# Performance work log

Hardware: AMD Instinct MI355X
Metric: run time of the kernel (lower is better)

## Reference

```python
import jax, jax.numpy as jnp
import numpy as np

B, N, M = 2, 4096, 12288
K, SH, H, GK, NC, F = 64, 32, 64, 8, 200, 1


def sph_to_cart(theta, phi):
    st = jnp.sin(theta)
    return jnp.stack([st * jnp.cos(phi), st * jnp.sin(phi), jnp.cos(theta)], axis=-1)


def setup_inputs() -> dict:
    key = jax.random.key(0)
    ks = jax.random.split(key, 16)
    theta = jax.random.uniform(ks[0], (B, N)) * jnp.pi
    phi = jax.random.uniform(ks[1], (B, N)) * 2 * jnp.pi
    feat = jax.random.normal(ks[2], (B, N))
    xxx = jnp.stack([theta, phi, feat], axis=1)  # [B,3,N]
    pt = jax.random.uniform(ks[3], (M,)) * jnp.pi
    pp = jax.random.uniform(ks[4], (M,)) * 2 * jnp.pi
    pix_theta_phi = jnp.stack([pt, pp], axis=1)  # [M,2]
    s = 0.1
    return dict(
        xxx=xxx,
        pix_theta_phi=pix_theta_phi,
        att_w1=jax.random.normal(ks[5], (F + 1, SH)) * s,
        att_b1=jnp.zeros((SH,)),
        att_w2=jax.random.normal(ks[6], (SH, 1)) * s,
        att_b2=jnp.zeros((1,)),
        proj_w=jax.random.normal(ks[7], (F, H)) * s,
        proj_b=jnp.zeros((H,)),
        rel_w=jax.random.normal(ks[8], (3, H, H)) * s,
        rel_b=jnp.zeros((3, H)),
        root_w=jax.random.normal(ks[9], (3, H, H)) * s,
        out_w1=jax.random.normal(ks[10], (H, H)) * s,
        out_b1=jnp.zeros((H,)),
        out_w2=jax.random.normal(ks[11], (H, NC)) * s,
        out_b2=jnp.zeros((NC,)),
    )


def reference(xxx, pix_theta_phi, att_w1, att_b1, att_w2, att_b2, proj_w, proj_b,
              rel_w, rel_b, root_w, out_w1, out_b1, out_w2, out_b2):
    # --- sparse healpix sampler ---
    los_tp = jnp.transpose(xxx[:, :2, :], (0, 2, 1))   # [B,N,2]
    x = xxx[:, 2, :][..., None]                        # [B,N,1]
    r_los = sph_to_cart(los_tp[..., 0], los_tp[..., 1])           # [B,N,3]
    r_pix = sph_to_cart(pix_theta_phi[:, 0], pix_theta_phi[:, 1])  # [M,3]
    cos = jnp.clip(jnp.einsum('bnc,mc->bmn', r_los, r_pix), -1.0, 1.0)  # [B,M,N]
    vals, idx = jax.lax.top_k(cos, K)                  # [B,M,K]
    x_g = jax.vmap(lambda xb, ib: xb[ib])(x, idx)      # [B,M,K,F]
    d = jnp.arccos(jnp.clip(vals, -1.0, 1.0))          # [B,M,K]
    feat = jnp.concatenate([x_g, d[..., None]], axis=-1)  # [B,M,K,F+1]
    logits = jax.nn.relu(feat @ att_w1 + att_b1) @ att_w2 + att_b2  # [B,M,K,1]
    w = jax.nn.softmax(logits[..., 0], axis=-1)        # [B,M,K]
    pooled = jnp.einsum('bmk,bmkf->bmf', w, x_g)       # [B,M,F]
    # --- GNN on healpix grid ---
    h = jax.nn.relu(pooled @ proj_w + proj_b)          # [B,M,H]
    m = r_pix.shape[0]
    sq = jnp.sum(r_pix * r_pix, axis=1)
    d2 = sq[:, None] + sq[None, :] - 2.0 * (r_pix @ r_pix.T)       # [M,M]
    d2 = jnp.where(jnp.eye(m, dtype=bool), jnp.inf, d2)  # loop=False
    _, nbr = jax.lax.top_k(-d2, GK)                    # [M,GK] knn_graph
    for i in range(rel_w.shape[0]):
        agg = h[:, nbr, :].sum(axis=2)                 # sum-aggregate neighbor msgs
        h = jax.nn.relu(agg @ rel_w[i] + rel_b[i] + h @ root_w[i])
    graph_feat = h.mean(axis=1)                        # global_mean_pool -> [B,H]
    out = jax.nn.relu(graph_feat @ out_w1 + out_b1) @ out_w2 + out_b2
    return out
```

## Files before the change

kernel.cpp:

```cpp
#include <hip/hip_runtime.h>
#include <hip/hip_bf16.h>

#define B_ 2
#define N_ 4096
#define M_ 12288
#define K_ 64
#define SH_ 32
#define H_ 64
#define GK_ 8
#define NC_ 200

#define SCAP 288
#define KCAP 240
#define MG_ 0.01f
#define C256_ 81.48733086f

static __device__ __forceinline__ unsigned f2key(float f) {
  unsigned b = __float_as_uint(f);
  return (b & 0x80000000u) ? ~b : (b | 0x80000000u);
}
static __device__ __forceinline__ float key2f(unsigned u) {
  unsigned b = (u & 0x80000000u) ? (u & 0x7fffffffu) : ~u;
  return __uint_as_float(b);
}
static __device__ __forceinline__ unsigned long long shflxor64(unsigned long long x, int m) {
  unsigned lo = (unsigned)x, hi = (unsigned)(x >> 32);
  lo = (unsigned)__shfl_xor((int)lo, m);
  hi = (unsigned)__shfl_xor((int)hi, m);
  return ((unsigned long long)hi << 32) | lo;
}
static __device__ __forceinline__ unsigned long long kpack(float s, int j) {
  return ((unsigned long long)f2key(s) << 14) | (unsigned)(16383 - j);
}
static __device__ __forceinline__ unsigned long long spack(float c, int n) {
  return ((unsigned long long)f2key(c) << 12) | (unsigned)(4095 - n);
}
static __device__ __forceinline__ int thbkt(float th) {
  int b = (int)(th * C256_);
  return b < 0 ? 0 : (b > 255 ? 255 : b);
}
static __device__ __forceinline__ float clamp1(float x) { return fminf(1.f, fmaxf(-1.f, x)); }
static __device__ __forceinline__ float rdlane(float v, int c) {
  return __uint_as_float((unsigned)__builtin_amdgcn_readlane((int)__float_as_uint(v), c));
}

__global__ __launch_bounds__(256) void sentinel_vA(float* out, int n, float val) {
  int t = blockIdx.x * 256 + threadIdx.x;
  if (t < n) out[t] = val;
}

#define THRB_ 6144
#define PREPN_ (M_ + B_*N_ + B_*H_)
#define PREPB_ ((PREPN_ + 255)/256)

__global__ __launch_bounds__(256) void prepthr_vA(
    const float* __restrict__ xxx, const float* __restrict__ pix,
    float4* __restrict__ r_pix, float4* __restrict__ r_los, float* __restrict__ gf,
    float* __restrict__ kthr, float* __restrict__ cthr, unsigned* __restrict__ cnt)
{
  const float PI = 3.14159265358979f;
  if ((int)blockIdx.x < THRB_) {
    int gid  = blockIdx.x*4 + (threadIdx.x >> 6);
    int lane = threadIdx.x & 63;
    int tgt  = (gid >= M_) ? 1 : 0;
    int row  = gid - tgt*M_;
    float thp = pix[2*row];
    float cp = cosf(thp), sp = fmaxf(sinf(thp), 1e-6f);
    float thq = ((float)lane + 0.5f) * (PI/64.f);
    float sq = sinf(thq), cq = cosf(thq);
    float rinv = 1.0f / (sq * sp);
    float At = tgt ? (2.f*PI*PI*192.f/(float)N_) : (2.f*PI*PI*128.f/(float)M_);
    float lo = 1e-3f, hi = 3.1414f;
    for (int it = 0; it < 12; ++it) {
      float al = 0.5f*(lo + hi);
      float ca = cosf(al);
      float arg = clamp1((ca - cq*cp) * rinv);
      float ax = fabsf(arg);
      float ac = sqrtf(fmaxf(0.f, 1.f - ax)) *
// ... 13 lines not shown
  } else {
    int tid = ((int)blockIdx.x - THRB_)*256 + threadIdx.x;
    if (tid < M_) {
      float th = pix[2*tid], ph = pix[2*tid+1];
      float st = sinf(th);
      float x = st*cosf(ph), y = st*sinf(ph), z = cosf(th);
      r_pix[tid] = make_float4(x, y, z, x*x + y*y + z*z);
      atomicAdd(&cnt[thbkt(th)], 1u);
    }
    int t2 = tid - M_;
    if (t2 >= 0 && t2 < B_*N_) {
      int b = t2 >> 12, n = t2 & (N_-1);
      const float* xb = xxx + b*3*N_;
      float th = xb[n], ph = xb[N_+n], ft = xb[2*N_+n];
      float st = sinf(th);
      r_los[t2] = make_float4(st*cosf(ph), st*sinf(ph), cosf(th), ft);
      atomicAdd(&cnt[256 + b*256 + thbkt(th)], 1u);
    }
    int t3 = tid - M_ - B_*N_;
    if (t3 >= 0 && t3 < B_*H_) gf[t3] = 0.0f;
  }
}

__global__ __launch_bounds__(256) void scan_vA(
    const unsigned* __restrict__ cnt, int* __restrict__ pstart, int* __restrict__ lstart,
    unsigned* __restrict__ pcur, unsigned* __restrict__ lcur)
{
  __shared__ unsigned buf[256];
  const int t = threadIdx.x;
  for (int arr = 0; arr < 3; ++arr) {
    unsigned v = cnt[arr*256 + t];
    buf[t] = v;
    __syncthreads();
    for (int off = 1; off < 256; off <<= 1) {
      unsigned o = (t >= off) ? buf[t - off] : 0u;
      __syncthreads();
      buf[t] += o;
      __syncthreads();
    }
    unsigned incl = buf[t], excl = incl - v;
    if (arr == 0) {
      pstart[t] = (int)excl; if (t == 255) pstart[256] = (int)incl;
      pcur[t] = excl;
    } else {
      int b = arr - 1;
      lstart[b*257 + t] = (int)excl; if (t == 255) lstart[b*257 + 256] = (int)incl;
      lcur[b*256 + t] = excl;
    }
    __syncthreads();
  }
}

__global__ __launch_bounds__(256) void scatter_vA(
    const float* __restrict__ xxx, const float* __restrict__ pix,
    const float4* __restrict__ r_pix, const float4* __restrict__ r_los,
    unsigned* __restrict__ pcur, unsigned* __restrict__ lcur,
    float4* __restrict__ spix, int* __restrict__ sjdx,
    float4* __restrict__ slos, int* __restrict__ sldx)
{
  int tid = blockIdx.x * 256 + threadIdx.x;
  if (tid < M_) {
    int bkt = thbkt(pix[2*tid]);
    unsigned pos = atomicAdd(&pcur[bkt], 1u);
    spix[pos] = r_pix[tid];
    sjdx[pos] = tid;
  } else {
    int t2 = tid - M_;
    if (t2 < B_*N_) {
      int b = t2 >> 12, n = t2 & (N_-1);
      int bkt = thbkt(xxx[b*3*N_ + n]);
      unsigned pos = atomicAdd(&lcur[b*256 + bkt], 1u);
      slos[b*N_ + pos] = r_los[t2];
      sldx[b*N_ + pos] = n;
    }
  }
}

__global__ __launch_bounds__(512) void sampler_vA(
    const float* __restrict__ pix,
    const float4* __restrict__ spix, const int* __restrict__ sjdx,
    const float4* __restrict__ slos, const int* __restrict__ sldx,
    const int* __restrict__ lstart, const float4* __restrict__ r_los,
    const float* __restrict__ cthr,
    const float* __restrict__ aw1, const float* __restrict__ ab1,
    const float* __restrict__ aw2, const float* __restrict__ ab2,
    float* __restrict__ pooled)
{
  __shared__ unsigned long long cKey[16][SCAP];
  __shared__ unsigned long long selKey[16][K_];
  __shared__ unsigned hist[16][64];
  __shared__ int bnd[16][16];

  const int tid = threadIdx.x, wv = tid >> 6, lane = tid & 63;
  const int b  = blockIdx.y;
  const int srow0 = blockIdx.x*16 + wv*2, srow1 = srow0 + 1;
  const int r0 = wv*2, r1 = r0 + 1;
  const int m0 = sjdx[srow0], m1 = sjdx[srow1];
  const float4 p0 = spix[srow0], p1 = spix[srow1];
  const float thp0 = pix[2*m0], thp1 = pix[2*m1];
  float th0 = cthr[m0], th1 = cthr[m1];
  const float inv0 = 63.999f / (1.000001f - th0);
  const float inv1 = 63.999f / (1.000001f - th1);
  const float4* sl = slos + b * N_;
  const int* sx = sldx + b * N_;
  const float4* rl = r_los + b * N_;
  const int* ls = lstart + b * 257;
  const unsigned long long ltm = (1ull << lane) - 1ull;

  hist[r0][lane] = 0u; hist[r1][lane] = 0u;

  unsigned cnt0 = 0, cnt1 = 0;
  {
    float al0 = acosf(clamp1(th0)), al1 = acosf(clamp1(th1));
    int blo = thbkt(fminf(thp0 - al0, thp1 - al1) - MG_);
    int bhi = thbkt(fmaxf(thp0 + al0, thp1 + al1) + MG_);
    int jlo = ls[blo], jhi = ls[bhi + 1];
    for (int base = jlo; base < jhi; base += 64) {
      int pos = base + lane;
      bool act = pos < jhi;
      float c0 = -2.f, c1 = -2.f; int n = 0;
      if (act) {
        float4 v = sl[pos]; n = sx[pos];
        c0 = clamp1(v.x*p0.x + v.y*p0.y + v.z*p0.z);
        c1 = clamp1(v.x*p1.x + v.y*p1.y + v.z*p1.z);
      }
      bool pr0 = c0 > th0, pr1 = c1 > th1;
      unsigned long long mk0 = __ballot(pr0);
      if (mk0) {
        unsigned off = (unsigned)__popcll(mk0 & ltm);
        if (pr0) {
          if (cnt0 + off < SCAP) cKey[r0][cnt0 + off] = spack(c0, n);
          atomicAdd(&hist[r0][(int)((c0 - th0) * inv0)], 1u);
        }
        cnt0 += (unsigned)__popcll(mk0);
      }
      unsigned long long mk1 = __ballot(pr1);
      if (mk1) {
        unsigned off = (unsigned)__popcll(mk1 & ltm);
        if (pr1) {
          if (cnt1 + off < SCAP) cKey[r1][cnt1 + off] = spack(c1, n);
          atomicAdd(&hist[r1][(int)((c1 - th1) * inv1)], 1u);
        }
        cnt1 += (unsigned)__popcll(mk1);
      }
    }
  }

  for (int rr = 0; rr < 2; ++rr) {
    const int r = (rr == 0) ? r0 : r1;
    const int m = (rr == 0) ? m0 : m1;
    const float4 p = (rr == 0) ? p0 : p1;
    const float thp = (rr == 0) ? thp0 : thp1;
    float th = (rr == 0) ? th0 : th1;
    float inv = (rr == 0) ? inv0 : inv1;
    unsigned cn = (rr == 0) ? cnt0 : cnt1;

    int tries = 0;
    while (cn < K_ && tries < 3) {
      th = 1.f - 1.6f*(1.f - th); ++tries;
      float al = acosf(clamp1(th));
      int blo = thbkt(thp - al - MG_), bhi = thbkt(thp + al + MG_);
      int jlo = ls[blo], jhi = ls[bhi + 1];
      cn = 0;
      for (int base = jlo; base < jhi; base += 64) {
        int pos = base + lane;
        bool act = pos < jhi;
        float c = -2.f; int n = 0;
        if (act) {
          float4 v = sl[pos]; n = sx[pos];
          c = clamp1(v.x*p.x + v.y*p.y + v.z*p.z);
        }
        bool pr = c > th;
        unsigned long long mk = __ballot(pr);
        if (mk) {
          unsigned off = (unsigned)__popcll(mk & ltm);
          if (pr && cn + off < SCAP) cKey[r][cn + off] = spack(c, n);
          cn += (unsigned)__popcll(mk);
        }
      }
    }

    if (cn < K_ || cn > SCAP) {
      unsigned long long prev = ~0ull;
      for (int rd = 0; rd < K_; ++rd) {
        unsigned long long best = 0ull;
        for (int i = 0; i < 64; ++i) {
          int n = lane + 64*i;
          float4 v = rl[n];
          float c = clamp1(v.x*p.x + v.y*p.y + v.z*p.z);
          unsigned long long k = spack(c, n);
          if (k < prev && k > best) best = k;
        }
        #pragma unroll
        for (int off = 1; off < 64; off <<= 1) {
          unsigned long long o = shflxor64(best, off);
          best = o > best ? o : best;
        }
        if (lane == 0) selKey[r][rd] = best;
        prev = best;
      }
    } else {
      if (tries > 0) {
        inv = 63.999f / (1.000001f - th);
        hist[r][lane] = 0u;
        for (unsigned base = 0; base < cn; base += 64) {
          unsigned it = base + lane;
          if (it < cn) {
            float c = key2f((unsigned)(cKey[r][it] >> 12));
            atomicAdd(&hist[r][(int)((c - th) * inv)], 1u);
          }
        }
      }
      unsigned g = hist[r][lane], s = g;
      #pragma unroll
      for (int off = 1; off < 64; off <<= 1) {
        unsigned t2 = (unsigned)__shfl_down((int)s, off);
        s += (lane + off < 64) ? t2 : 0u;
      }
      unsigned snext = s - g;
      unsigned packed = (s >= K_ && snext < K_) ? (((unsigned)(lane+1) << 16) | snext) : 0u;
      #pragma unroll
      for (int off = 32; off; off >>= 1) {
        unsigned o = (unsigned)__shfl_xor((int)packed, off);
        packed = packed > o ? packed : o;
      }
      const int t = (int)(packed >> 16) - 1;
      const unsigned chi = packed & 0xFFFFu;
      const unsigned need = K_ - chi;
      unsigned hiC = 0, bdC = 0;
      for (unsigned base = 0; base < cn; base += 64) {
        unsigned it = base + lane;
        bool act = it < cn;
        unsigned long long key = act ? cKey[r][it] : 0ull;
        int bin = -1;
        if (act) bin = (int)((key2f((unsigned)(key >> 12)) - th) * inv);
        bool pHi = act && bin > t;
        bool pBd = act && bin == t;
        unsigned long long mH = __ballot(pHi);
        unsigned offH = (unsigned)__popcll(mH & ltm);
        if (pHi && hiC + offH < K_) selKey[r][hiC + offH] = key;
        hiC += (unsigned)__popcll(mH);
        unsigned long long mB = __ballot(pBd);
        unsigned offB = (unsigned)__popcll(mB & ltm);
        if (pBd && bdC + offB < 16u) bnd[r][bdC + offB] = (int)it;
        bdC += (unsigned)__popcll(mB);
      }
      if (bdC <= 16u) {
        if (lane < (int)bdC) {
          unsigned long long ki = cKey[r][bnd[r][lane]];
          int rank = 0;
          for (int j = 0; j < (int)bdC; ++j) rank += (cKey[r][bnd[r][j]] > ki) ? 1 : 0;
          if ((unsigned)rank < need) selKey[r][chi + rank] = ki;
        }
      } else {
        for (unsigned base = 0; base < cn; base += 64) {
          unsigned it = base + lane;
          if (it < cn) {
            unsigned long long ki = cKey[r][it];
            int bin = (int)((key2f((unsigned)(ki >> 12)) - th) * inv);
            if (bin == t) {
              int rank = 0;
              for (unsigned j = 0; j < cn; ++j) {
                unsigned long long kj = cKey[r][j];
                int bj = (int)((key2f((unsigned)(kj >> 12)) - th) * inv);
                rank += (bj == t && kj > ki) ? 1 : 0;
              }
              if ((unsigned)rank < need) selKey[r][chi + rank] = ki;
            }
          }
        }
      }
    }

    {
      unsigned long long key = selKey[r][lane];
      int n = 4095 - (int)(key & 0xFFFull);
      float c = key2f((unsigned)(key >> 12));
      float xg = rl[n].w;
      float d  = acosf(clamp1(c));
      float acc = ab2[0];
      for (int s2 = 0; s2 < SH_; ++s2)
        acc += fmaxf(xg*aw1[s2] + d*aw1[SH_+s2] + ab1[s2], 0.f) * aw2[s2];
      float mx = acc;
      #pragma unroll
      for (int off = 32; off; off >>= 1) mx = fmaxf(mx, __shfl_xor(mx, off));
      float e = expf(acc - mx);
      float se = e, sxe = e * xg;
      #pragma unroll
      for (int off = 32; off; off >>= 1) { se += __shfl_xor(se, off); sxe += __shfl_xor(sxe, off); }
      if (lane == 0) pooled[b*M_ + m] = sxe / se;
    }
  }
}

__global__ __launch_bounds__(512) void knn_vA(
    const float* __restrict__ pix,
    const float4* __restrict__ spix, const int* __restrict__ sjdx,
    const int* __restrict__ pstart, const float4* __restrict__ r_pix,
    const float* __restrict__ kthr, int* __restrict__ nbr)
{
  __shared__ unsigned long long cKey[16][KCAP];

  const int tid = threadIdx.x, wv = tid >> 6, lane = tid & 63;
  const int lr0 = wv*2;
  const int srow0 = blockIdx.x*16 + lr0, srow1 = srow0 + 1;
  const int i0 = sjdx[srow0], i1 = sjdx[srow1];
  const float4 p0 = spix[srow0], p1 = spix[srow1];
  const float thp0 = pix[2*i0], thp1 = pix[2*i1];
  const float t0 = kthr[i0], t1 = kthr[i1];
  const unsigned long long ltm = (1ull << lane) - 1ull;

  unsigned cnt0 = 0, cnt1 = 0;
  {
    float al0 = acosf(clamp1((t0 + 1.00002f)*0.5f));
    float al1 = acosf(clamp1((t1 + 1.00002f)*0.5f));
    int blo = thbkt(fminf(thp0 - al0, thp1 - al1) - MG_);
    int bhi = thbkt(fmaxf(thp0 + al0, thp1 + al1) + MG_);
    int jlo = pstart[blo], jhi = pstart[bhi + 1];
    for (int base = jlo; base < jhi; base += 64) {
      int pos = base + lane;
      bool act = pos < jhi;
      float s0 = -1e30f, s1 = -1e30f; int j = -1;
      if (act) {
        float4 v = spix[pos]; j = sjdx[pos];
        s0 = 2.f*(p0.x*v.x + p0.y*v.y + p0.z*v.z) - v.w;
        s1 = 2.f*(p1.x*v.x + p1.y*v.y + p1.z*v.z) - v.w;
      }
      bool pr0 = act && (j != i0) && (s0 > t0);
      bool pr1 = act && (j != i1) && (s1 > t1);
      unsigned long long mk0 = __ballot(pr0);
      if (mk0) {
        unsigned off = (unsigned)__popcll(mk0 & ltm);
        if (pr0 && cnt0 + off < KCAP) cKey[lr0][cnt0 + off] = kpack(s0, j);
        cnt0 += (unsigned)__popcll(mk0);
      }
      unsigned long long mk1 = __ballot(pr1);
      if (mk1) {
        unsigned off = (unsigned)__popcll(mk1 & ltm);
        if (pr1 && cnt1 + off < KCAP) cKey[lr0+1][cnt1 + off] = kpack(s1, j);
        cnt1 += (unsigned)__popcll(mk1);
      }
    }
  }

  for (int rr = 0; rr < 2; ++rr) {
    const int lr = lr0 + rr;
    const int i  = (rr == 0) ? i0 : i1;
    const float4 pi = (rr == 0) ? p0 : p1;
    const float thp = (rr == 0) ? thp0 : thp1;
    float th = (rr == 0) ? t0 : t1;
    unsigned cn = (rr == 0) ? cnt0 : cnt1;

    int tries = 0;
    while (cn < (unsigned)GK_ && tries < 3) {
      th = 1.6f*th - 0.6f; ++tries;
      float al = acosf(clamp1((th + 1.00002f)*0.5f));
      int blo = thbkt(thp - al - MG_), bhi = thbkt(thp + al + MG_);
      int jlo = pstart[blo], jhi = pstart[bhi + 1];
      cn = 0;
      for (int base = jlo; base < jhi; base += 64) {
        int pos = base + lane;
        bool act = pos < jhi;
        float s = -1e30f; int j = -1;
        if (act) {
          float4 v = spix[pos]; j = sjdx[pos];
          s = 2.f*(pi.x*v.x + pi.y*v.y + pi.z*v.z) - v.w;
        }
        bool pr = act && (j != i) && (s > th);
        unsigned long long mk = __ballot(pr);
        if (mk) {
          unsigned off = (unsigned)__popcll(mk & ltm);
          if (pr && cn + off < KCAP) cKey[lr][cn + off] = kpack(s, j);
          cn += (unsigned)__popcll(mk);
        }
      }
    }

    if (cn >= (unsigned)GK_ && cn <= (unsigned)KCAP) {
      unsigned long long pk[4];
      #pragma unroll
      for (int t2 = 0; t2 < 4; ++t2) {
        int idx = lane + 64*t2;
        pk[t2] = (idx < (int)cn) ? cKey[lr][idx] : 0ull;
      }
      for (int round = 0; round < GK_; ++round) {
        unsigned long long loc = pk[0]; int lt = 0;
        #pragma unroll
        for (int t2 = 1; t2 < 4; ++t2) if (pk[t2] > loc) { loc = pk[t2]; lt = t2; }
        unsigned long long best = loc;
        #pragma unroll
        for (int off = 1; off < 64; off <<= 1) {
          unsigned long long o = shflxor64(best, off);
          best = o > best ? o : best;
        }
        if (loc == best) {
          #pragma unroll
          for (int t2 = 0; t2 < 4; ++t2) if (t2 == lt) pk[t2] = 0ull;
        }
        if (lane == round) nbr[i*GK_ + round] = 16383 - (int)(best & 16383ull);
      }
    } else {
      unsigned long long prev = ~0ull;
      for (int rd = 0; rd < GK_; ++rd) {
        unsigned long long best = 0ull;
        for (int j = lane; j < M_; j += 64) {
          float4 v = r_pix[j];
          float s = 2.f*(pi.x*v.x + pi.y*v.y + pi.z*v.z) - v.w;
          if (j != i) {
            unsigned long long k = kpack(s, j);
            if (k < prev && k > best) best = k;
          }
        }
        #pragma unroll
        for (int off = 1; off < 64; off <<= 1) {
          unsigned long long o = shflxor64(best, off);
          best = o > best ? o : best;
        }
        if (lane == rd) nbr[i*GK_ + rd] = 16383 - (int)(best & 16383ull);
        prev = best;
      }
    }
  }
}

__global__ __launch_bounds__(256) void gnn1f_vA(
    const float* __restrict__ pooled, float* __restrict__ hout, const int* __restrict__ nbr,
    const float* __restrict__ pw, const float* __restrict__ pb,
    const float* __restrict__ relw, const float* __restrict__ relb,
    const float* __restrict__ rootw)
{
  __shared__ float wrel[H_*H_], wroot[H_*H_];
  const int tid = threadIdx.x;
  #pragma unroll
  for (int q = 0; q < 16; ++q) {
    int idx = tid + 256*q;
    wrel[idx]  = relw[idx];
    wroot[idx] = rootw[idx];
  }
  __syncthreads();

  const int lane = tid & 63;
  const int wave = tid >> 6;
  const int b = blockIdx.y;
  const int m0 = blockIdx.x * 16 + wave * 4;
  const float* pldb = pooled + (size_t)b * M_;
  const float pwl = pw[lane], pbl = pb[lane], rbl = relb[lane];

  float h[4], agg[4], acc[4];
// ... 5 lines not shown
    float a = 0.f;
    #pragma unroll
    for (int k = 0; k < GK_; ++k) {
      int nb = nbr[m*GK_ + k];
      nb = nb < 0 ? 0 : (nb >= M_ ? M_-1 : nb);
      float pn = pldb[nb];
      a += fmaxf(pn*pwl + pbl, 0.f);
    }
    agg[t] = a;
    acc[t] = rbl;
  }
  #pragma unroll
  for (int c = 0; c < H_; ++c) {
    float wr = wrel[c*H_ + lane], wo = wroot[c*H_ + lane];
    #pragma unroll
    for (int t = 0; t < 4; ++t)
      acc[t] += rdlane(agg[t], c) * wr + rdlane(h[t], c) * wo;
  }
  #pragma unroll
  for (int t = 0; t < 4; ++t)
    hout[((size_t)b*M_ + m0 + t)*H_ + lane] = fmaxf(acc[t], 0.f);
}

__global__ __launch_bounds__(256) void gnn_vA(
    const float* __restrict__ hin, float* __restrict__ hout, const int* __restrict__ nbr,
    const float* __restrict__ relw, const float* __restrict__ relb,
    const float* __restrict__ rootw)
{
  __shared__ float wrel[H_*H_], wroot[H_*H_];
  const int tid = threadIdx.x;
  #pragma unroll
  for (int q = 0; q < 16; ++q) {
    int idx = tid + 256*q;
    wrel[idx]  = relw[idx];
    wroot[idx] = rootw[idx];
  }
  __syncthreads();

  const int lane = tid & 63;
  const int wave = tid >> 6;
  const int b = blockIdx.y;
  const int m0 = blockIdx.x * 16 + wave * 4;
  const float* hb = hin + (size_t)b * M_ * H_;
  const float rbl = relb[lane];

  float h[4], agg[4], acc[4];
  #pragma unroll
// ... 2 lines not shown
    h[t] = hb[m*H_ + lane];
    float a = 0.f;
    #pragma unroll
    for (int k = 0; k < GK_; ++k) {
      int nb = nbr[m*GK_ + k];
      nb = nb < 0 ? 0 : (nb >= M_ ? M_-1 : nb);
      a += hb[nb*H_ + lane];
    }
    agg[t] = a;
    acc[t] = rbl;
  }
  #pragma unroll
  for (int c = 0; c < H_; ++c) {
    float wr = wrel[c*H_ + lane], wo = wroot[c*H_ + lane];
    #pragma unroll
    for (int t = 0; t < 4; ++t)
      acc[t] += rdlane(agg[t], c) * wr + rdlane(h[t], c) * wo;
  }
  #pragma unroll
  for (int t = 0; t < 4; ++t)
    hout[((size_t)b*M_ + m0 + t)*H_ + lane] = fmaxf(acc[t], 0.f);
}

__global__ __launch_bounds__(256) void gnn3r_vA(
    const float* __restrict__ hin, float* __restrict__ gf, const int* __restrict__ nbr,
    const float* __restrict__ relw, const float* __restrict__ relb,
    const float* __restrict__ rootw)
{
  __shared__ float wrel[H_*H_], wroot[H_*H_];
  __shared__ float gacc[H_];
  const int tid = threadIdx.x;
  #pragma unroll
  for (int q = 0; q < 16; ++q) {
    int idx = tid + 256*q;
    wrel[idx]  = relw[idx];
    wroot[idx] = rootw[idx];
  }
  if (tid < H_) gacc[tid] = 0.f;
  __syncthreads();

  const int lane = tid & 63;
  const int wave = tid >> 6;
  const int b = blockIdx.y;
  const int m0 = blockIdx.x * 16 + wave * 4;
  const float* hb = hin + (size_t)b * M_ * H_;
  const float rbl = relb[lane];

// ... 5 lines not shown
    float a = 0.f;
    #pragma unroll
    for (int k = 0; k < GK_; ++k) {
      int nb = nbr[m*GK_ + k];
      nb = nb < 0 ? 0 : (nb >= M_ ? M_-1 : nb);
      a += hb[nb*H_ + lane];
    }
    agg[t] = a;
    acc[t] = rbl;
  }
  #pragma unroll
  for (int c = 0; c < H_; ++c) {
    float wr = wrel[c*H_ + lane], wo = wroot[c*H_ + lane];
    #pragma unroll
    for (int t = 0; t < 4; ++t)
      acc[t] += rdlane(agg[t], c) * wr + rdlane(h[t], c) * wo;
  }
  float ps = fmaxf(acc[0], 0.f) + fmaxf(acc[1], 0.f) + fmaxf(acc[2], 0.f) + fmaxf(acc[3], 0.f);
  atomicAdd(&gacc[lane], ps);
  __syncthreads();
  if (tid < H_) atomicAdd(&gf[b*H_ + tid], gacc[tid]);
}

__global__ __launch_bounds__(256) void head_vA(
    const float* __restrict__ gf, const float* __restrict__ w1,
    const float* __restrict__ b1, const float* __restrict__ w2,
    const float* __restrict__ b2, float* __restrict__ out)
{
  __shared__ float gfm[B_][H_], hid[B_][H_];
  const int tid = threadIdx.x;
  if (tid < B_*H_) gfm[tid >> 6][tid & 63] = gf[tid] * (1.f / (float)M_);
  __syncthreads();
  if (tid < B_*H_) {
    int b = tid >> 6, j = tid & 63;
    float acc = b1[j];
    for (int c = 0; c < H_; ++c) acc += gfm[b][c] * w1[c*H_ + j];
    hid[b][j] = fmaxf(acc, 0.f);
  }
  __syncthreads();
  for (int t = tid; t < B_*NC_; t += 256) {
    int b = t / NC_, o = t - b*NC_;
    float acc = b2[o];
    for (int j = 0; j < H_; ++j) acc += hid[b][j] * w2[j*NC_ + o];
    out[t] = acc;
  }
}

extern "C" void kernel_launch(void* const* d_in, const int* in_sizes, int n_in,
                              void* d_out, int out_size, void* d_ws, size_t ws_size,
                              hipStream_t stream)
{
  float* out = (float*)d_out;

  const size_t need = (size_t)M_*16 + (size_t)B_*N_*16 + (size_t)B_*M_*4
                    + (size_t)M_*GK_*4 + 2*(size_t)B_*M_*H_*4 + (size_t)B_*H_*4;
  bool ok_ws = ws_size >= need;
  bool ok_in = (n_in == 15) && (out_size == B_*NC_)
            && in_sizes[0] == B_*3*N_ && in_sizes[1] == M_*2
            && in_sizes[2] == 2*SH_ && in_sizes[5] == 1
            && in_sizes[8] == 3*H_*H_ && in_sizes[13] == H_*NC_;
  if (!ok_ws || !ok_in) {
    sentinel_vA<<<(out_size + 255)/256, 256, 0, stream>>>(out, out_size, ok_in ? 42.f : 43.f);
    return;
  }

  const float* xxx    = (const float*)d_in[0];
  const float* pix    = (const float*)d_in[1];
  const float* att_w1 = (const float*)d_in[2];
  const float* att_b1 = (const float*)d_in[3];
  const float* att_w2 = (const float*)d_in[4];
  const float* att_b2 = (const float*)d_in[5];
  const float* proj_w = (const float*)d_in[6];
  const float* proj_b = (const float*)d_in[7];
  const float* rel_w  = (const float*)d_in[8];
  const float* rel_b  = (const float*)d_in[9];
  const float* root_w = (const float*)d_in[10];
  const float* out_w1 = (const float*)d_in[11];
  const float* out_b1 = (const float*)d_in[12];
  const float* out_w2 = (const float*)d_in[13];
  const float* out_b2 = (const float*)d_in[14];

  char* w = (char*)d_ws;
  float4* r_pix = (float4*)w;  w += (size_t)M_ * 16;
  float4* r_los = (float4*)w;  w += (size_t)B_ * N_ * 16;
  float*  pooled = (float*)w;  w += (size_t)B_ * M_ * 4;
  int*    nbr = (int*)w;       w += (size_t)M_ * GK_ * 4;
  float*  h0 = (float*)w;      w += (size_t)B_ * M_ * H_ * 4;
  float*  h1 = (float*)w;      w += (size_t)B_ * M_ * H_ * 4;
  float*  gf = (float*)w;      w += (size_t)B_ * H_ * 4;

  float*  kthr = h0;
  float*  cthr = h0 + M_;
  float4* spix = (float4*)(h0 + 2*M_);
  int*    sjdx = (int*)(h0 + 6*M_);
  float4* slos = (float4*)(h0 + 7*M_);
  int*    sldx = (int*)(h0 + 7*M_ + 4*B_*N_);
  unsigned* cnt = (unsigned*)(h0 + 7*M_ + 5*B_*N_);
  int*    pstart = (int*)(cnt + 768);
  int*    lstart = pstart + 257;
  unsigned* pcur = (unsigned*)(lstart + 514);
  unsigned* lcur = pcur + 256;

  hipMemsetAsync(cnt, 0, 768*sizeof(unsigned), stream);
  prepthr_vA<<<THRB_ + PREPB_, 256, 0, stream>>>(xxx, pix, r_pix, r_los, gf, kthr, cthr, cnt);
  scan_vA<<<1, 256, 0, stream>>>(cnt, pstart, lstart, pcur, lcur);
  scatter_vA<<<(M_ + B_*N_ + 255)/256, 256, 0, stream>>>(xxx, pix, r_pix, r_los, pcur, lcur,
                                                         spix, sjdx, slos, sldx);
  sampler_vA<<<dim3(M_/16, B_), 512, 0, stream>>>(pix, spix, sjdx, slos, sldx, lstart, r_los,
                                                  cthr, att_w1, att_b1, att_w2, att_b2, pooled);
  knn_vA<<<M_/16, 512, 0, stream>>>(pix, spix, sjdx, pstart, r_pix, kthr, nbr);
  gnn1f_vA<<<dim3(M_/16, B_), 256, 0, stream>>>(pooled, h1, nbr, proj_w, proj_b,
                                                rel_w + 0*H_*H_, rel_b + 0*H_, root_w + 0*H_*H_);
  gnn_vA<<<dim3(M_/16, B_), 256, 0, stream>>>(h1, h0, nbr, rel_w + 1*H_*H_, rel_b + 1*H_, root_w + 1*H_*H_);
  gnn3r_vA<<<dim3(M_/16, B_), 256, 0, stream>>>(h0, gf, nbr, rel_w + 2*H_*H_, rel_b + 2*H_, root_w + 2*H_*H_);
  head_vA<<<1, 256, 0, stream>>>(gf, out_w1, out_b1, out_w2, out_b2, out);
}
```

Measured before the change: 275.3 us.

## Fuse sampler and kNN kernels into one launch with block-kind dispatch

```diff
diff --git a/kernel.cpp b/kernel.cpp
--- a/kernel.cpp
+++ b/kernel.cpp
@@ -44,7 +44,7 @@
   return __uint_as_float((unsigned)__builtin_amdgcn_readlane((int)__float_as_uint(v), c));
 }
 
-__global__ __launch_bounds__(256) void sentinel_vA(float* out, int n, float val) {
+__global__ __launch_bounds__(256) void sentinel_vB(float* out, int n, float val) {
   int t = blockIdx.x * 256 + threadIdx.x;
   if (t < n) out[t] = val;
 }
@@ -53,7 +53,7 @@
 #define PREPN_ (M_ + B_*N_ + B_*H_)
 #define PREPB_ ((PREPN_ + 255)/256)
 
-__global__ __launch_bounds__(256) void prepthr_vA(
+__global__ __launch_bounds__(256) void prepthr_vB(
     const float* __restrict__ xxx, const float* __restrict__ pix,
     float4* __restrict__ r_pix, float4* __restrict__ r_los, float* __restrict__ gf,
     float* __restrict__ kthr, float* __restrict__ cthr, unsigned* __restrict__ cnt)
@@ -113,7 +113,7 @@
   }
 }
 
-__global__ __launch_bounds__(256) void scan_vA(
+__global__ __launch_bounds__(256) void scan_vB(
     const unsigned* __restrict__ cnt, int* __restrict__ pstart, int* __restrict__ lstart,
     unsigned* __restrict__ pcur, unsigned* __restrict__ lcur)
 {
@@ -142,7 +142,7 @@
   }
 }
 
-__global__ __launch_bounds__(256) void scatter_vA(
+__global__ __launch_bounds__(256) void scatter_vB(
     const float* __restrict__ xxx, const float* __restrict__ pix,
     const float4* __restrict__ r_pix, const float4* __restrict__ r_los,
     unsigned* __restrict__ pcur, unsigned* __restrict__ lcur,
@@ -167,354 +167,340 @@
   }
 }
 
-__global__ __launch_bounds__(512) void sampler_vA(
+__global__ __launch_bounds__(512) void samknn_vB(
     const float* __restrict__ pix,
     const float4* __restrict__ spix, const int* __restrict__ sjdx,
     const float4* __restrict__ slos, const int* __restrict__ sldx,
-    const int* __restrict__ lstart, const float4* __restrict__ r_los,
-    const float* __restrict__ cthr,
+    const int* __restrict__ lstart, const int* __restrict__ pstart,
+    const float4* __restrict__ r_pix, const float4* __restrict__ r_los,
+    const float* __restrict__ cthr, const float* __restrict__ kthr,
     const float* __restrict__ aw1, const float* __restrict__ ab1,
     const float* __restrict__ aw2, const float* __restrict__ ab2,
-    float* __restrict__ pooled)
-{
-  __shared__ unsigned long long cKey[16][SCAP];
-  __shared__ unsigned long long selKey[16][K_];
-  __shared__ unsigned hist[16][64];
-  __shared__ int bnd[16][16];
+    float* __restrict__ pooled, int* __restrict__ nbr)
+{
+  __shared__ unsigned long long smem[6272];
 
   const int tid = threadIdx.x, wv = tid >> 6, lane = tid & 63;
-  const int b  = blockIdx.y;
-  const int srow0 = blockIdx.x*16 + wv*2, srow1 = srow0 + 1;
-  const int r0 = wv*2, r1 = r0 + 1;
-  const int m0 = sjdx[srow0], m1 = sjdx[srow1];
-  const float4 p0 = spix[srow0], p1 = spix[srow1];
-  const float thp0 = pix[2*m0], thp1 = pix[2*m1];
-  float th0 = cthr[m0], th1 = cthr[m1];
-  const float inv0 = 63.999f / (1.000001f - th0);
-  const float inv1 = 63.999f / (1.000001f - th1);
-  const float4* sl = slos + b * N_;
-  const int* sx = sldx + b * N_;
-  const float4* rl = r_los + b * N_;
-  const int* ls = lstart + b * 257;
+  const int kind = blockIdx.x % 3;
+  const int grp  = blockIdx.x / 3;
   const unsigned long long ltm = (1ull << lane) - 1ull;
 
-  hist[r0][lane] = 0u; hist[r1][lane] = 0u;
-
-  unsigned cnt0 = 0, cnt1 = 0;
-  {
-    float al0 = acosf(clamp1(th0)), al1 = acosf(clamp1(th1));
-    int blo = thbkt(fminf(thp0 - al0, thp1 - al1) - MG_);
-    int bhi = thbkt(fmaxf(thp0 + al0, thp1 + al1) + MG_);
-    int jlo = ls[blo], jhi = ls[bhi + 1];
-    for (int base = jlo; base < jhi; base += 64) {
-      int pos = base + lane;
-      bool act = pos < jhi;
-      float c0 = -2.f, c1 = -2.f; int n = 0;
-      if (act) {
-        float4 v = sl[pos]; n = sx[pos];
-        c0 = clamp1(v.x*p0.x + v.y*p0.y + v.z*p0.z);
-        c1 = clamp1(v.x*p1.x + v.y*p1.y + v.z*p1.z);
-      }
-      bool pr0 = c0 > th0, pr1 = c1 > th1;
-      unsigned long long mk0 = __ballot(pr0);
-      if (mk0) {
-        unsigned off = (unsigned)__popcll(mk0 & ltm);
-        if (pr0) {
-          if (cnt0 + off < SCAP) cKey[r0][cnt0 + off] = spack(c0, n);
-          atomicAdd(&hist[r0][(int)((c0 - th0) * inv0)], 1u);
-        }
-        cnt0 += (unsigned)__popcll(mk0);
-      }
-      unsigned long long mk1 = __ballot(pr1);
-      if (mk1) {
-        unsigned off = (unsigned)__popcll(mk1 & ltm);
-        if (pr1) {
-          if (cnt1 + off < SCAP) cKey[r1][cnt1 + off] = spack(c1, n);
-          atomicAdd(&hist[r1][(int)((c1 - th1) * inv1)], 1u);
-        }
-        cnt1 += (unsigned)__popcll(mk1);
-      }
-    }
-  }
-
-  for (int rr = 0; rr < 2; ++rr) {
-    const int r = (rr == 0) ? r0 : r1;
-    const int m = (rr == 0) ? m0 : m1;
-    const float4 p = (rr == 0) ? p0 : p1;
-    const float thp = (rr == 0) ? thp0 : thp1;
-    float th = (rr == 0) ? th0 : th1;
-    float inv = (rr == 0) ? inv0 : inv1;
-    unsigned cn = (rr == 0) ? cnt0 : cnt1;
-
-    int tries = 0;
-    while (cn < K_ && tries < 3) {
-      th = 1.f - 1.6f*(1.f - th); ++tries;
-      float al = acosf(clamp1(th));
-      int blo = thbkt(thp - al - MG_), bhi = thbkt(thp + al + MG_);
+  if (kind < 2) {
+    unsigned long long* cKey   = smem;
+    unsigned long long* selKey = smem + 16*SCAP;
+    unsigned* hist = (unsigned*)(smem + 16*SCAP + 16*64);
+    int* bnd = (int*)(hist + 16*64);
+
+    const int b = kind;
+    const int srow0 = grp*16 + wv*2, srow1 = srow0 + 1;
+    const int r0 = wv*2, r1 = r0 + 1;
+    const int m0 = sjdx[srow0], m1 = sjdx[srow1];
+    const float4 p0 = spix[srow0], p1 = spix[srow1];
+    const float thp0 = pix[2*m0], thp1 = pix[2*m1];
+    float th0 = cthr[m0], th1 = cthr[m1];
+    const float4* sl = slos + b * N_;
+    const int* sx = sldx + b * N_;
+    const float4* rl = r_los + b * N_;
+    const int* ls = lstart + b * 257;
+
+    unsigned cnt0 = 0, cnt1 = 0;
+    {
+      float al0 = acosf(clamp1(th0)), al1 = acosf(clamp1(th1));
+      int blo = thbkt(fminf(thp0 - al0, thp1 - al1) - MG_);
+      int bhi = thbkt(fmaxf(thp0 + al0, thp1 + al1) + MG_);
       int jlo = ls[blo], jhi = ls[bhi + 1];
-      cn = 0;
       for (int base = jlo; base < jhi; base += 64) {
         int pos = base + lane;
         bool act = pos < jhi;
-        float c = -2.f; int n = 0;
+        float c0 = -2.f, c1 = -2.f; int n = 0;
         if (act) {
           float4 v = sl[pos]; n = sx[pos];
-          c = clamp1(v.x*p.x + v.y*p.y + v.z*p.z);
-        }
-        bool pr = c > th;
-        unsigned long long mk = __ballot(pr);
-        if (mk) {
-          unsigned off = (unsigned)__popcll(mk & ltm);
-          if (pr && cn + off < SCAP) cKey[r][cn + off] = spack(c, n);
-          cn += (unsigned)__popcll(mk);
+          c0 = clamp1(v.x*p0.x + v.y*p0.y + v.z*p0.z);
+          c1 = clamp1(v.x*p1.x + v.y*p1.y + v.z*p1.z);
+        }
+        bool pr0 = c0 > th0, pr1 = c1 > th1;
+        unsigned long long mk0 = __ballot(pr0);
+        if (mk0) {
+          unsigned off = (unsigned)__popcll(mk0 & ltm);
+          if (pr0 && cnt0 + off < SCAP) cKey[r0*SCAP + cnt0 + off] = spack(c0, n);
+          cnt0 += (unsigned)__popcll(mk0);
+        }
+        unsigned long long mk1 = __ballot(pr1);
+        if (mk1) {
+          unsigned off = (unsigned)__popcll(mk1 & ltm);
+          if (pr1 && cnt1 + off < SCAP) cKey[r1*SCAP + cnt1 + off] = spack(c1, n);
+          cnt1 += (unsigned)__popcll(mk1);
         }
       }
     }
 
-    if (cn < K_ || cn > SCAP) {
-      unsigned long long prev = ~0ull;
-      for (int rd = 0; rd < K_; ++rd) {
-        unsigned long long best = 0ull;
-        for (int i = 0; i < 64; ++i) {
-          int n = lane + 64*i;
-          float4 v = rl[n];
-          float c = clamp1(v.x*p.x + v.y*p.y + v.z*p.z);
-          unsigned long long k = spack(c, n);
-          if (k < prev && k > best) best = k;
-        }
-        #pragma unroll
-        for (int off = 1; off < 64; off <<= 1) {
-          unsigned long long o = shflxor64(best, off);
-          best = o > best ? o : best;
-        }
-        if (lane == 0) selKey[r][rd] = best;
-        prev = best;
+    for (int rr = 0; rr < 2; ++rr) {
+      const int r = (rr == 0) ? r0 : r1;
+      const int m = (rr == 0) ? m0 : m1;
+      const float4 p = (rr == 0) ? p0 : p1;
+      const float thp = (rr == 0) ? thp0 : thp1;
+      float th = (rr == 0) ? th0 : th1;
+      unsigned cn = (rr == 0) ? cnt0 : cnt1;
+
+      int tries = 0;
+      while (cn < K_ && tries < 3) {
+        th = 1.f - 1.6f*(1.f - th); ++tries;
+        float al = acosf(clamp1(th));
+        int blo = thbkt(thp - al - MG_), bhi = thbkt(thp + al + MG_);
+        int jlo = ls[blo], jhi = ls[bhi + 1];
+        cn = 0;
+        for (int base = jlo; base < jhi; base += 64) {
+          int pos = base + lane;
+          bool act = pos < jhi;
+          float c = -2.f; int n = 0;
+          if (act) {
+            float4 v = sl[pos]; n = sx[pos];
+            c = clamp1(v.x*p.x + v.y*p.y + v.z*p.z);
+          }
+          bool pr = c > th;
+          unsigned long long mk = __ballot(pr);
+          if (mk) {
+            unsigned off = (unsigned)__popcll(mk & ltm);
+            if (pr && cn + off < SCAP) cKey[r*SCAP + cn + off] = spack(c, n);
+            cn += (unsigned)__popcll(mk);
+          }
+        }
       }
-    } else {
-      if (tries > 0) {
-        inv = 63.999f / (1.000001f - th);
-        hist[r][lane] = 0u;
+
+      if (cn < K_ || cn > SCAP) {
+        unsigned long long prev = ~0ull;
+        for (int rd = 0; rd < K_; ++rd) {
+          unsigned long long best = 0ull;
+          for (int i = 0; i < 64; ++i) {
+            int n = lane + 64*i;
+            float4 v = rl[n];
+            float c = clamp1(v.x*p.x + v.y*p.y + v.z*p.z);
+            unsigned long long k = spack(c, n);
+            if (k < prev && k > best) best = k;
+          }
+          #pragma unroll
+          for (int off = 1; off < 64; off <<= 1) {
+            unsigned long long o = shflxor64(best, off);
+            best = o > best ? o : best;
+          }
+          if (lane == 0) selKey[r*64 + rd] = best;
+          prev = best;
+        }
+      } else {
+        const float inv = 63.999f / (1.000001f - th);
+        hist[r*64 + lane] = 0u;
         for (unsigned base = 0; base < cn; base += 64) {
           unsigned it = base + lane;
           if (it < cn) {
-            float c = key2f((unsigned)(cKey[r][it] >> 12));
-            atomicAdd(&hist[r][(int)((c - th) * inv)], 1u);
-          }
-        }
-      }
-      unsigned g = hist[r][lane], s = g;
-      #pragma unroll
-      for (int off = 1; off < 64; off <<= 1) {
-        unsigned t2 = (unsigned)__shfl_down((int)s, off);
-        s += (lane + off < 64) ? t2 : 0u;
-      }
-      unsigned snext = s - g;
-      unsigned packed = (s >= K_ && snext < K_) ? (((unsigned)(lane+1) << 16) | snext) : 0u;
-      #pragma unroll
-      for (int off = 32; off; off >>= 1) {
-        unsigned o = (unsigned)__shfl_xor((int)packed, off);
-        packed = packed > o ? packed : o;
-      }
-      const int t = (int)(packed >> 16) - 1;
-      const unsigned chi = packed & 0xFFFFu;
-      const unsigned need = K_ - chi;
-      unsigned hiC = 0, bdC = 0;
-      for (unsigned base = 0; base < cn; base += 64) {
-        unsigned it = base + lane;
-        bool act = it < cn;
-        unsigned long long key = act ? cKey[r][it] : 0ull;
-        int bin = -1;
-        if (act) bin = (int)((key2f((unsigned)(key >> 12)) - th) * inv);
-        bool pHi = act && bin > t;
-        bool pBd = act && bin == t;
-        unsigned long long mH = __ballot(pHi);
-        unsigned offH = (unsigned)__popcll(mH & ltm);
-        if (pHi && hiC + offH < K_) selKey[r][hiC + offH] = key;
-        hiC += (unsigned)__popcll(mH);
-        unsigned long long mB = __ballot(pBd);
-        unsigned offB = (unsigned)__popcll(mB & ltm);
-        if (pBd && bdC + offB < 16u) bnd[r][bdC + offB] = (int)it;
-        bdC += (unsigned)__popcll(mB);
-      }
-      if (bdC <= 16u) {
-        if (lane < (int)bdC) {
-          unsigned long long ki = cKey[r][bnd[r][lane]];
-          int rank = 0;
-          for (int j = 0; j < (int)bdC; ++j) rank += (cKey[r][bnd[r][j]] > ki) ? 1 : 0;
-          if ((unsigned)rank < need) selKey[r][chi + rank] = ki;
-        }
-      } else {
+            float c = key2f((unsigned)(cKey[r*SCAP + it] >> 12));
+            atomicAdd(&hist[r*64 + (int)((c - th) * inv)], 1u);
+          }
+        }
+        unsigned g = hist[r*64 + lane], s = g;
+        #pragma unroll
+        for (int off = 1; off < 64; off <<= 1) {
+          unsigned t2 = (unsigned)__shfl_down((int)s, off);
+          s += (lane + off < 64) ? t2 : 0u;
+        }
+        unsigned snext = s - g;
+        unsigned packed = (s >= K_ && snext < K_) ? (((unsigned)(lane+1) << 16) | snext) : 0u;
+        #pragma unroll
+        for (int off = 32; off; off >>= 1) {
+          unsigned o = (unsigned)__shfl_xor((int)packed, off);
+          packed = packed > o ? packed : o;
+        }
+        const int t = (int)(packed >> 16) - 1;
+        const unsigned chi = packed & 0xFFFFu;
+        const unsigned need = K_ - chi;
+        unsigned hiC = 0, bdC = 0;
         for (unsigned base = 0; base < cn; base += 64) {
           unsigned it = base + lane;
-          if (it < cn) {
-            unsigned long long ki = cKey[r][it];
-            int bin = (int)((key2f((unsigned)(ki >> 12)) - th) * inv);
-            if (bin == t) {
-              int rank = 0;
-              for (unsigned j = 0; j < cn; ++j) {
-                unsigned long long kj = cKey[r][j];
-                int bj = (int)((key2f((unsigned)(kj >> 12)) - th) * inv);
-                rank += (bj == t && kj > ki) ? 1 : 0;
+          bool act = it < cn;
+          unsigned long long key = act ? cKey[r*SCAP + it] : 0ull;
+          int bin = -1;
+          if (act) bin = (int)((key2f((unsigned)(key >> 12)) - th) * inv);
+          bool pHi = act && bin > t;
+          bool pBd = act && bin == t;
+          unsigned long long mH = __ballot(pHi);
+          unsigned offH = (unsigned)__popcll(mH & ltm);
+          if (pHi && hiC + offH < K_) selKey[r*64 + hiC + offH] = key;
+          hiC += (unsigned)__popcll(mH);
+          unsigned long long mB = __ballot(pBd);
+          unsigned offB = (unsigned)__popcll(mB & ltm);
+          if (pBd && bdC + offB < 16u) bnd[r*16 + bdC + offB] = (int)it;
+          bdC += (unsigned)__popcll(mB);
+        }
+        if (bdC <= 16u) {
+          if (lane < (int)bdC) {
+            unsigned long long ki = cKey[r*SCAP + bnd[r*16 + lane]];
+            int rank = 0;
+            for (int j = 0; j < (int)bdC; ++j) rank += (cKey[r*SCAP + bnd[r*16 + j]] > ki) ? 1 : 0;
+            if ((unsigned)rank < need) selKey[r*64 + chi + rank] = ki;
+          }
+        } else {
+          for (unsigned base = 0; base < cn; base += 64) {
+            unsigned it = base + lane;
+            if (it < cn) {
+              unsigned long long ki = cKey[r*SCAP + it];
+              int bin = (int)((key2f((unsigned)(ki >> 12)) - th) * inv);
+              if (bin == t) {
+                int rank = 0;
+                for (unsigned j = 0; j < cn; ++j) {
+                  unsigned long long kj = cKey[r*SCAP + j];
+                  int bj = (int)((key2f((unsigned)(kj >> 12)) - th) * inv);
+                  rank += (bj == t && kj > ki) ? 1 : 0;
+                }
+                if ((unsigned)rank < need) selKey[r*64 + chi + rank] = ki;
               }
-              if ((unsigned)rank < need) selKey[r][chi + rank] = ki;
             }
           }
         }
       }
-    }
-
+
+      {
+        unsigned long long key = selKey[r*64 + lane];
+        int n = 4095 - (int)(key & 0xFFFull);
+        float c = key2f((unsigned)(key >> 12));
+        float xg = rl[n].w;
+        float d  = acosf(clamp1(c));
+        float acc = ab2[0];
+        for (int s2 = 0; s2 < SH_; ++s2)
+          acc += fmaxf(xg*aw1[s2] + d*aw1[SH_+s2] + ab1[s2], 0.f) * aw2[s2];
+        float mx = acc;
+        #pragma unroll
+        for (int off = 32; off; off >>= 1) mx = fmaxf(mx, __shfl_xor(mx, off));
+        float e = expf(acc - mx);
+        float se = e, sxe = e * xg;
+        #pragma unroll
+        for (int off = 32; off; off >>= 1) { se += __shfl_xor(se, off); sxe += __shfl_xor(sxe, off); }
+        if (lane == 0) pooled[b*M_ + m] = sxe / se;
+      }
+    }
+  } else {
+    unsigned long long* cKey = smem;
+
+    const int lr0 = wv*2;
+    const int srow0 = grp*16 + lr0, srow1 = srow0 + 1;
+    const int i0 = sjdx[srow0], i1 = sjdx[srow1];
+    const float4 p0 = spix[srow0], p1 = spix[srow1];
+    const float thp0 = pix[2*i0], thp1 = pix[2*i1];
+    const float t0 = kthr[i0], t1 = kthr[i1];
+
+    unsigned cnt0 = 0, cnt1 = 0;
     {
-      unsigned long long key = selKey[r][lane];
-      int n = 4095 - (int)(key & 0xFFFull);
-      float c = key2f((unsigned)(key >> 12));
-      float xg = rl[n].w;
-      float d  = acosf(clamp1(c));
-      float acc = ab2[0];
-      for (int s2 = 0; s2 < SH_; ++s2)
-        acc += fmaxf(xg*aw1[s2] + d*aw1[SH_+s2] + ab1[s2], 0.f) * aw2[s2];
-      float mx = acc;
-      #pragma unroll
-      for (int off = 32; off; off >>= 1) mx = fmaxf(mx, __shfl_xor(mx, off));
-      float e = expf(acc - mx);
-      float se = e, sxe = e * xg;
-      #pragma unroll
-      for (int off = 32; off; off >>= 1) { se += __shfl_xor(se, off); sxe += __shfl_xor(sxe, off); }
-      if (lane == 0) pooled[b*M_ + m] = sxe / se;
-    }
-  }
-}
-
-__global__ __launch_bounds__(512) void knn_vA(
-    const float* __restrict__ pix,
-    const float4* __restrict__ spix, const int* __restrict__ sjdx,
-    const int* __restrict__ pstart, const float4* __restrict__ r_pix,
-    const float* __restrict__ kthr, int* __restrict__ nbr)
-{
-  __shared__ unsigned long long cKey[16][KCAP];
-
-  const int tid = threadIdx.x, wv = tid >> 6, lane = tid & 63;
-  const int lr0 = wv*2;
-  const int srow0 = blockIdx.x*16 + lr0, srow1 = srow0 + 1;
-  const int i0 = sjdx[srow0], i1 = sjdx[srow1];
-  const float4 p0 = spix[srow0], p1 = spix[srow1];
-  const float thp0 = pix[2*i0], thp1 = pix[2*i1];
-  const float t0 = kthr[i0], t1 = kthr[i1];
-  const unsigned long long ltm = (1ull << lane) - 1ull;
-
-  unsigned cnt0 = 0, cnt1 = 0;
-  {
-    float al0 = acosf(clamp1((t0 + 1.00002f)*0.5f));
-    float al1 = acosf(clamp1((t1 + 1.00002f)*0.5f));
-    int blo = thbkt(fminf(thp0 - al0, thp1 - al1) - MG_);
-    int bhi = thbkt(fmaxf(thp0 + al0, thp1 + al1) + MG_);
-    int jlo = pstart[blo], jhi = pstart[bhi + 1];
-    for (int base = jlo; base < jhi; base += 64) {
-      int pos = base + lane;
-      bool act = pos < jhi;
-      float s0 = -1e30f, s1 = -1e30f; int j = -1;
-      if (act) {
-        float4 v = spix[pos]; j = sjdx[pos];
-        s0 = 2.f*(p0.x*v.x + p0.y*v.y + p0.z*v.z) - v.w;
-        s1 = 2.f*(p1.x*v.x + p1.y*v.y + p1.z*v.z) - v.w;
-      }
-      bool pr0 = act && (j != i0) && (s0 > t0);
-      bool pr1 = act && (j != i1) && (s1 > t1);
-      unsigned long long mk0 = __ballot(pr0);
-      if (mk0) {
-        unsigned off = (unsigned)__popcll(mk0 & ltm);
-        if (pr0 && cnt0 + off < KCAP) cKey[lr0][cnt0 + off] = kpack(s0, j);
-        cnt0 += (unsigned)__popcll(mk0);
-      }
-      unsigned long long mk1 = __ballot(pr1);
-      if (mk1) {
-        unsigned off = (unsigned)__popcll(mk1 & ltm);
-        if (pr1 && cnt1 + off < KCAP) cKey[lr0+1][cnt1 + off] = kpack(s1, j);
-        cnt1 += (unsigned)__popcll(mk1);
-      }
-    }
-  }
-
-  for (int rr = 0; rr < 2; ++rr) {
-    const int lr = lr0 + rr;
-    const int i  = (rr == 0) ? i0 : i1;
-    const float4 pi = (rr == 0) ? p0 : p1;
-    const float thp = (rr == 0) ? thp0 : thp1;
-    float th = (rr == 0) ? t0 : t1;
-    unsigned cn = (rr == 0) ? cnt0 : cnt1;
-
-    int tries = 0;
-    while (cn < (unsigned)GK_ && tries < 3) {
-      th = 1.6f*th - 0.6f; ++tries;
-      float al = acosf(clamp1((th + 1.00002f)*0.5f));
-      int blo = thbkt(thp - al - MG_), bhi = thbkt(thp + al + MG_);
+      float al0 = acosf(clamp1((t0 + 1.00002f)*0.5f));
+      float al1 = acosf(clamp1((t1 + 1.00002f)*0.5f));
+      int blo = thbkt(fminf(thp0 - al0, thp1 - al1) - MG_);
+      int bhi = thbkt(fmaxf(thp0 + al0, thp1 + al1) + MG_);
       int jlo = pstart[blo], jhi = pstart[bhi + 1];
-      cn = 0;
       for (int base = jlo; base < jhi; base += 64) {
         int pos = base + lane;
         bool act = pos < jhi;
-        float s = -1e30f; int j = -1;
+        float s0 = -1e30f, s1 = -1e30f; int j = -1;
         if (act) {
           float4 v = spix[pos]; j = sjdx[pos];
-          s = 2.f*(pi.x*v.x + pi.y*v.y + pi.z*v.z) - v.w;
-        }
-        bool pr = act && (j != i) && (s > th);
-        unsigned long long mk = __ballot(pr);
-        if (mk) {
-          unsigned off = (unsigned)__popcll(mk & ltm);
-          if (pr && cn + off < KCAP) cKey[lr][cn + off] = kpack(s, j);
-          cn += (unsigned)__popcll(mk);
+          s0 = 2.f*(p0.x*v.x + p0.y*v.y + p0.z*v.z) - v.w;
+          s1 = 2.f*(p1.x*v.x + p1.y*v.y + p1.z*v.z) - v.w;
+        }
+        bool pr0 = act && (j != i0) && (s0 > t0);
+        bool pr1 = act && (j != i1) && (s1 > t1);
+        unsigned long long mk0 = __ballot(pr0);
+        if (mk0) {
+          unsigned off = (unsigned)__popcll(mk0 & ltm);
+          if (pr0 && cnt0 + off < KCAP) cKey[lr0*KCAP + cnt0 + off] = kpack(s0, j);
+          cnt0 += (unsigned)__popcll(mk0);
+        }
+        unsigned long long mk1 = __ballot(pr1);
+        if (mk1) {
+          unsigned off = (unsigned)__popcll(mk1 & ltm);
+          if (pr1 && cnt1 + off < KCAP) cKey[(lr0+1)*KCAP + cnt1 + off] = kpack(s1, j);
+          cnt1 += (unsigned)__popcll(mk1);
         }
       }
     }
 
-    if (cn >= (unsigned)GK_ && cn <= (unsigned)KCAP) {
-      unsigned long long pk[4];
-      #pragma unroll
-      for (int t2 = 0; t2 < 4; ++t2) {
-        int idx = lane + 64*t2;
-        pk[t2] = (idx < (int)cn) ? cKey[lr][idx] : 0ull;
+    for (int rr = 0; rr < 2; ++rr) {
+      const int lr = lr0 + rr;
+      const int i  = (rr == 0) ? i0 : i1;
+      const float4 pi = (rr == 0) ? p0 : p1;
+      const float thp = (rr == 0) ? thp0 : thp1;
+      float th = (rr == 0) ? t0 : t1;
+      unsigned cn = (rr == 0) ? cnt0 : cnt1;
+
+      int tries = 0;
+      while (cn < (unsigned)GK_ && tries < 3) {
+        th = 1.6f*th - 0.6f; ++tries;
+        float al = acosf(clamp1((th + 1.00002f)*0.5f));
+        int blo = thbkt(thp - al - MG_), bhi = thbkt(thp + al + MG_);
+        int jlo = pstart[blo], jhi = pstart[bhi + 1];
+        cn = 0;
+        for (int base = jlo; base < jhi; base += 64) {
+          int pos = base + lane;
+          bool act = pos < jhi;
+          float s = -1e30f; int j = -1;
+          if (act) {
+            float4 v = spix[pos]; j = sjdx[pos];
+            s = 2.f*(pi.x*v.x + pi.y*v.y + pi.z*v.z) - v.w;
+          }
+          bool pr = act && (j != i) && (s > th);
+          unsigned long long mk = __ballot(pr);
+          if (mk) {
+            unsigned off = (unsigned)__popcll(mk & ltm);
+            if (pr && cn + off < KCAP) cKey[lr*KCAP + cn + off] = kpack(s, j);
+            cn += (unsigned)__popcll(mk);
+          }
+        }
       }
-      for (int round = 0; round < GK_; ++round) {
-        unsigned long long loc = pk[0]; int lt = 0;
+
+      if (cn >= (unsigned)GK_ && cn <= (unsigned)KCAP) {
+        unsigned long long pk[4];
         #pragma unroll
-        for (int t2 = 1; t2 < 4; ++t2) if (pk[t2] > loc) { loc = pk[t2]; lt = t2; }
-        unsigned long long best = loc;
-        #pragma unroll
-        for (int off = 1; off < 64; off <<= 1) {
-          unsigned long long o = shflxor64(best, off);
-          best = o > best ? o : best;
-        }
-        if (loc == best) {
+        for (int t2 = 0; t2 < 4; ++t2) {
+          int idx = lane + 64*t2;
+          pk[t2] = (idx < (int)cn) ? cKey[lr*KCAP + idx] : 0ull;
+        }
+        for (int round = 0; round < GK_; ++round) {
+          unsigned long long loc = pk[0]; int lt = 0;
           #pragma unroll
-          for (int t2 = 0; t2 < 4; ++t2) if (t2 == lt) pk[t2] = 0ull;
-        }
-        if (lane == round) nbr[i*GK_ + round] = 16383 - (int)(best & 16383ull);
+          for (int t2 = 1; t2 < 4; ++t2) if (pk[t2] > loc) { loc = pk[t2]; lt = t2; }
+          unsigned long long best = loc;
+          #pragma unroll
+          for (int off = 1; off < 64; off <<= 1) {
+            unsigned long long o = shflxor64(best, off);
+            best = o > best ? o : best;
+          }
+          if (loc == best) {
+            #pragma unroll
+            for (int t2 = 0; t2 < 4; ++t2) if (t2 == lt) pk[t2] = 0ull;
+          }
+          if (lane == round) nbr[i*GK_ + round] = 16383 - (int)(best & 16383ull);
+        }
+      } else {
+        unsigned long long prev = ~0ull;
+        for (int rd = 0; rd < GK_; ++rd) {
+          unsigned long long best = 0ull;
+          for (int j = lane; j < M_; j += 64) {
+            float4 v = r_pix[j];
+            float s = 2.f*(pi.x*v.x + pi.y*v.y + pi.z*v.z) - v.w;
+            if (j != i) {
+              unsigned long long k = kpack(s, j);
+              if (k < prev && k > best) best = k;
+            }
+          }
+          #pragma unroll
+          for (int off = 1; off < 64; off <<= 1) {
+            unsigned long long o = shflxor64(best, off);
+            best = o > best ? o : best;
+          }
+          if (lane == rd) nbr[i*GK_ + rd] = 16383 - (int)(best & 16383ull);
+          prev = best;
+        }
       }
-    } else {
-      unsigned long long prev = ~0ull;
-      for (int rd = 0; rd < GK_; ++rd) {
-        unsigned long long best = 0ull;
-        for (int j = lane; j < M_; j += 64) {
-          float4 v = r_pix[j];
-          float s = 2.f*(pi.x*v.x + pi.y*v.y + pi.z*v.z) - v.w;
-          if (j != i) {
-            unsigned long long k = kpack(s, j);
-            if (k < prev && k > best) best = k;
-          }
-        }
-        #pragma unroll
-        for (int off = 1; off < 64; off <<= 1) {
-          unsigned long long o = shflxor64(best, off);
-          best = o > best ? o : best;
-        }
-        if (lane == rd) nbr[i*GK_ + rd] = 16383 - (int)(best & 16383ull);
-        prev = best;
-      }
-    }
-  }
-}
-
-__global__ __launch_bounds__(256) void gnn1f_vA(
+    }
+  }
+}
+
+__global__ __launch_bounds__(256) void gnn1f_vB(
     const float* __restrict__ pooled, float* __restrict__ hout, const int* __restrict__ nbr,
     const float* __restrict__ pw, const float* __restrict__ pb,
     const float* __restrict__ relw, const float* __restrict__ relb,
@@ -566,7 +552,7 @@
     hout[((size_t)b*M_ + m0 + t)*H_ + lane] = fmaxf(acc[t], 0.f);
 }
 
-__global__ __launch_bounds__(256) void gnn_vA(
+__global__ __launch_bounds__(256) void gnn_vB(
     const float* __restrict__ hin, float* __restrict__ hout, const int* __restrict__ nbr,
     const float* __restrict__ relw, const float* __restrict__ relb,
     const float* __restrict__ rootw)
@@ -615,7 +601,7 @@
     hout[((size_t)b*M_ + m0 + t)*H_ + lane] = fmaxf(acc[t], 0.f);
 }
 
-__global__ __launch_bounds__(256) void gnn3r_vA(
+__global__ __launch_bounds__(256) void gnn3r_vB(
     const float* __restrict__ hin, float* __restrict__ gf, const int* __restrict__ nbr,
     const float* __restrict__ relw, const float* __restrict__ relb,
     const float* __restrict__ rootw)
@@ -667,7 +653,7 @@
   if (tid < H_) atomicAdd(&gf[b*H_ + tid], gacc[tid]);
 }
 
-__global__ __launch_bounds__(256) void head_vA(
+__global__ __launch_bounds__(256) void head_vB(
     const float* __restrict__ gf, const float* __restrict__ w1,
     const float* __restrict__ b1, const float* __restrict__ w2,
     const float* __restrict__ b2, float* __restrict__ out)
@@ -705,7 +691,7 @@
             && in_sizes[2] == 2*SH_ && in_sizes[5] == 1
             && in_sizes[8] == 3*H_*H_ && in_sizes[13] == H_*NC_;
   if (!ok_ws || !ok_in) {
-    sentinel_vA<<<(out_size + 255)/256, 256, 0, stream>>>(out, out_size, ok_in ? 42.f : 43.f);
+    sentinel_vB<<<(out_size + 255)/256, 256, 0, stream>>>(out, out_size, ok_in ? 42.f : 43.f);
     return;
   }
 
@@ -747,16 +733,16 @@
   unsigned* lcur = pcur + 256;
 
   hipMemsetAsync(cnt, 0, 768*sizeof(unsigned), stream);
-  prepthr_vA<<<THRB_ + PREPB_, 256, 0, stream>>>(xxx, pix, r_pix, r_los, gf, kthr, cthr, cnt);
-  scan_vA<<<1, 256, 0, stream>>>(cnt, pstart, lstart, pcur, lcur);
-  scatter_vA<<<(M_ + B_*N_ + 255)/256, 256, 0, stream>>>(xxx, pix, r_pix, r_los, pcur, lcur,
+  prepthr_vB<<<THRB_ + PREPB_, 256, 0, stream>>>(xxx, pix, r_pix, r_los, gf, kthr, cthr, cnt);
+  scan_vB<<<1, 256, 0, stream>>>(cnt, pstart, lstart, pcur, lcur);
+  scatter_vB<<<(M_ + B_*N_ + 255)/256, 256, 0, stream>>>(xxx, pix, r_pix, r_los, pcur, lcur,
                                                          spix, sjdx, slos, sldx);
-  sampler_vA<<<dim3(M_/16, B_), 512, 0, stream>>>(pix, spix, sjdx, slos, sldx, lstart, r_los,
-                                                  cthr, att_w1, att_b1, att_w2, att_b2, pooled);
-  knn_vA<<<M_/16, 512, 0, stream>>>(pix, spix, sjdx, pstart, r_pix, kthr, nbr);
-  gnn1f_vA<<<dim3(M_/16, B_), 256, 0, stream>>>(pooled, h1, nbr, proj_w, proj_b,
+  samknn_vB<<<3*(M_/16), 512, 0, stream>>>(pix, spix, sjdx, slos, sldx, lstart, pstart,
+                                           r_pix, r_los, cthr, kthr,
+                                           att_w1, att_b1, att_w2, att_b2, pooled, nbr);
+  gnn1f_vB<<<dim3(M_/16, B_), 256, 0, stream>>>(pooled, h1, nbr, proj_w, proj_b,
                                                 rel_w + 0*H_*H_, rel_b + 0*H_, root_w + 0*H_*H_);
-  gnn_vA<<<dim3(M_/16, B_), 256, 0, stream>>>(h1, h0, nbr, rel_w + 1*H_*H_, rel_b + 1*H_, root_w + 1*H_*H_);
-  gnn3r_vA<<<dim3(M_/16, B_), 256, 0, stream>>>(h0, gf, nbr, rel_w + 2*H_*H_, rel_b + 2*H_, root_w + 2*H_*H_);
-  head_vA<<<1, 256, 0, stream>>>(gf, out_w1, out_b1, out_w2, out_b2, out);
-}
+  gnn_vB<<<dim3(M_/16, B_), 256, 0, stream>>>(h1, h0, nbr, rel_w + 1*H_*H_, rel_b + 1*H_, root_w + 1*H_*H_);
+  gnn3r_vB<<<dim3(M_/16, B_), 256, 0, stream>>>(h0, gf, nbr, rel_w + 2*H_*H_, rel_b + 2*H_, root_w + 2*H_*H_);
+  head_vB<<<1, 256, 0, stream>>>(gf, out_w1, out_b1, out_w2, out_b2, out);
+}
```

Result: slower. 294.0 us (+6.8%).
